# Kernel tuning notes

Measured on AMD Instinct MI355X. Metric: run time of the kernel, lower is better.

Reference implementation:

```python
import jax, jax.numpy as jnp
import numpy as np

S = 4096          # seq_len (longformer-large-4096)
H = 1024          # hidden_size
FF = 3072         # ffnn_size (hardcoded)
G = 100           # number of gold mentions
MAX_SPAN = 30     # max_span_length
TOP_LAMBDA = 0.2
LN_EPS = 1e-5
MASK_VAL = 10000.0


def setup_inputs() -> dict:
    key = jax.random.key(0)
    ks = jax.random.split(key, 16)
    sc = 0.02
    sequence_output = jax.random.normal(ks[0], (1, S, H), jnp.float32)
    attention_mask = jnp.ones((1, S), jnp.int32)
    # valid gold spans: 1 <= start <= end < start + MAX_SPAN (so torch's >0 filter keeps all)
    gs = jax.random.randint(ks[1], (G,), 1, S - MAX_SPAN)
    gl = jax.random.randint(ks[2], (G,), 0, MAX_SPAN)
    gold_mentions = jnp.stack([gs, gs + gl], axis=1).astype(jnp.int32)  # [G, 2]
    inp = {
        'sequence_output': sequence_output,
        'attention_mask': attention_mask,
        'gold_mentions': gold_mentions,
        # start_mention_mlp
        'W_sm': jax.random.normal(ks[3], (H, FF), jnp.float32) * sc,
        'b_sm': jnp.zeros((FF,), jnp.float32),
        'g_sm': jnp.ones((FF,), jnp.float32),
        'beta_sm': jnp.zeros((FF,), jnp.float32),
        # end_mention_mlp
        'W_em': jax.random.normal(ks[4], (H, FF), jnp.float32) * sc,
        'b_em': jnp.zeros((FF,), jnp.float32),
        'g_em': jnp.ones((FF,), jnp.float32),
        'beta_em': jnp.zeros((FF,), jnp.float32),
        # classifiers
        'w_start': jax.random.normal(ks[5], (FF,), jnp.float32) * sc,
        'b_start': jnp.zeros((), jnp.float32),
        'w_end': jax.random.normal(ks[6], (FF,), jnp.float32) * sc,
        'b_end': jnp.zeros((), jnp.float32),
        'W_s2e': jax.random.normal(ks[7], (FF, FF), jnp.float32) * sc,
        'b_s2e': jnp.zeros((FF,), jnp.float32),
    }
    return inp


def _fcl(x, W, b, g, beta):
    # dense -> gelu (exact) -> layernorm (dropout is identity in eval)
    h = jax.nn.gelu(x @ W + b, approximate=False)
    mu = jnp.mean(h, axis=-1, keepdims=True)
    var = jnp.mean(jnp.square(h - mu), axis=-1, keepdims=True)
    return (h - mu) * jax.lax.rsqrt(var + LN_EPS) * g + beta


def _forward(sequence_output, attention_mask, gold_mentions,
             W_sm, b_sm, g_sm, beta_sm, W_em, b_em, g_em, beta_em,
             w_start, b_start, w_end, b_end, W_s2e, b_s2e):
    start_reps = _fcl(sequence_output, W_sm, b_sm, g_sm, beta_sm)  # [1,S,FF]
    end_reps = _fcl(sequence_output, W_em, b_em, g_em, beta_em)    # [1,S,FF]

    start_logits = jnp.einsum('bsf,f->bs', start_reps, w_start) + b_start  # [1,S]
    end_logits = jnp.einsum('bsf,f->bs', end_reps, w_end) + b_end          # [1,S]
    temp = start_reps @ W_s2e + b_s2e                                      # [1,S,FF]
    joint = jnp.einsum('bsf,btf->bst', temp, end_reps)                     # [1,S,S]
    mention_logits = joint + start_logits[:, :, None] + end_logits[:, None, :]

    # span mask: start <= end < start + MAX_SPAN (triu(0) then tril(MAX_SPAN-1))
    i = jnp.arange(S)
    mention_mask = ((i[:, None] <= i[None, :]) & (i[None, :] < i[:, None] + MAX_SPAN)
                    ).astype(jnp.float32)[None]  # [1,S,S]
    mention_logits = jnp.clip(mention_logits + (1.0 - mention_mask) * (-MASK_VAL),
                              -MASK_VAL, MASK_VAL)

    # top-k pruning; attention_mask is full so k is static: int(S * 0.2)
    max_k = int(S * TOP_LAMBDA)  # 819
    _, topk_1d = jax.lax.top_k(mention_logits.reshape(1, -1), max_k)  # [1,max_k]
    sorted_idx = jnp.sort(topk_1d, axis=-1)
    topk_start_ids = sorted_idx // S
    topk_end_ids = sorted_idx % S
    span_mask = jnp.ones((1, max_k), jnp.float32)

    # losses
    probs = jax.nn.sigmoid(mention_logits)  # [1,S,S]
    gstart = gold_mentions[:, 0]
    gend = gold_mentions[:, 1]
    gold_probs = probs[0, gstart, gend]
    # torch BCE clamps log at -100
    cost_gold = -jnp.mean(jnp.maximum(jnp.log(gold_probs), -100.0))
    junk = probs.at[0, gstart, gend].set(0.0)
    log1mp = jnp.maximum(jnp.log(1.0 - junk), -100.0)
    cost_junk = -jnp.sum(jnp.where(mention_mask == 1.0, log1mp, 0.0)) / jnp.sum(mention_mask)
    cost_is_mention = (cost_gold + cost_junk)[None]  # [1]

    return topk_start_ids, topk_end_ids, span_mask, sequence_output, cost_is_mention


def reference(sequence_output, attention_mask, gold_mentions,
              W_sm, b_sm, g_sm, beta_sm, W_em, b_em, g_em, beta_em,
              w_start, b_start, w_end, b_end, W_s2e, b_s2e):
    return _forward(sequence_output, attention_mask, gold_mentions,
                    W_sm, b_sm, g_sm, beta_sm, W_em, b_em, g_em, beta_em,
                    w_start, b_start, w_end, b_end, W_s2e, b_s2e)
```

## Files before the change

### kernel.cpp

```cpp
#include <hip/hip_runtime.h>
#include <math.h>

#define S 4096
#define H 1024
#define FF 3072
#define G 100
#define MAXSPAN 30
#define MAXK 819
#define NBAND (S * MAXSPAN)
#define BAND_COUNT 122445.0

#define O_START 0
#define O_END   819
#define O_MASK  1638
#define O_SEQ   2457
#define O_COST  (2457 + S * H)

typedef __bf16 bf16x8 __attribute__((ext_vector_type(8)));
typedef float f32x16 __attribute__((ext_vector_type(16)));


__device__ __forceinline__ float block_reduce_256(float x, volatile float* red) {
  #pragma unroll
  for (int off = 32; off > 0; off >>= 1) x += __shfl_down(x, off, 64);
  int wid = threadIdx.x >> 6;
  int lane = threadIdx.x & 63;
  __syncthreads();
  if (lane == 0) red[wid] = x;
  __syncthreads();
  return red[0] + red[1] + red[2] + red[3];
}

__device__ __forceinline__ float block_reduce_1024(float x, volatile float* red) {
  #pragma unroll
  for (int off = 32; off > 0; off >>= 1) x += __shfl_down(x, off, 64);
  int wid = threadIdx.x >> 6;
  int lane = threadIdx.x & 63;
  __syncthreads();
  if (lane == 0) red[wid] = x;
  __syncthreads();
  float s = 0.f;
  #pragma unroll
  for (int q = 0; q < 16; q++) s += red[q];
  return s;
}

__device__ __forceinline__ unsigned f2key(float f) {
  unsigned b = __float_as_uint(f);
  return (b & 0x80000000u) ? ~b : (b | 0x80000000u);
}

__device__ __forceinline__ unsigned short bf16_rne(float x) {
  unsigned u = __float_as_uint(x);
  unsigned r = ((u >> 16) & 1u) + 0x7FFFu;
  return (unsigned short)((u + r) >> 16);
}

__device__ __forceinline__ void split2(float x, unsigned short& h, unsigned short& l) {
  h = bf16_rne(x);
  float hf = __uint_as_float(((unsigned)h) << 16);
  l = bf16_rne(x - hf);
}

__device__ __forceinline__ void gld16(const void* g, void* l) {
  __builtin_amdgcn_global_load_lds(
      (const __attribute__((address_space(1))) unsigned int*)g,
      (__attribute__((address_space(3))) unsigned int*)l, 16, 0, 0);
}


__device__ __forceinline__ void pack_a_body(const float* __restrict__ A,
                                            float* __restrict__ Aout,
                                            unsigned short* __restrict__ hi,
                                            unsigned short* __restrict__ lo,
                                            int K, int bx, int by) {
  __shared__ float tile[32][33];
  const int t = threadIdx.x;
  const int tx = t & 31, ty8 = t >> 5;
  const int k0 = bx * 32, r0 = by * 32;
  #pragma unroll
  for (int r = ty8; r < 32; r += 8) {
    float v = A[(size_t)(r0 + r) * K + k0 + tx];
    tile[r][tx] = v;
    if (Aout) Aout[(size_t)(r0 + r) * K + k0 + tx] = v;
  }
  __syncthreads();
  if (t < 128) {
    const int kql = t >> 5;
    const int rl = t & 31;
    unsigned short h8[8], l8[8];
    #pragma unroll
    for (int s = 0; s < 8; s++) split2(tile[rl][kql * 8 + s], h8[s], l8[s]);
    const size_t panel = (size_t)(r0 >> 7);
    const int rloc = (r0 & 127) + rl;
    const size_t off = panel * (size_t)(128 * K) + (size_t)(k0 / 8 + kql) * 1024 + (size_t)rloc * 8;
    *(uint4*)(hi + off) = *(const uint4*)h8;
    *(uint4*)(lo + off) = *(const uint4*)l8;
  }
}

__device__ __forceinline__ void pack_ln_a_body(const float* __restrict__ A,
                                               const float* __restrict__ mu,
                                               const float* __restrict__ rstd,
                                               const float* __restrict__ g,
                                               const float* __restrict__ beta,
                                               unsigned short* __restrict__ hi,
                                               unsigned short* __restrict__ lo,
                                               int K, int bx, int by) {
  __shared__ float tile[32][33];
  const int t = threadIdx.x;
  const int tx = t & 31, ty8 = t >> 5;
  const int k0 = bx * 32, r0 = by * 32;
  #pragma unroll
  for (int r = ty8; r < 32; r += 8)
    tile[r][tx] = A[(size_t)(r0 + r) * K + k0 + tx];
  __syncthreads();
  if (t < 128) {
    const int kql = t >> 5;
    const int rl = t & 31;
    const int row = r0 + rl;
    const float m = mu[row], rs = rstd[row];
    float4 g0 = *(const float4*)(g + k0 + kql * 8);
    float4 g1 = *(const float4*)(g + k0 + kql * 8 + 4);
    float4 b0 = *(const float4*)(beta + k0 + kql * 8);
    float4 b1 = *(const float4*)(beta + k0 + kql * 8 + 4);
    float gv[8] = {g0.x, g0.y, g0.z, g0.w, g1.x, g1.y, g1.z, g1.w};
    float bv[8] = {b0.x, b0.y, b0.z, b0.w, b1.x, b1.y, b1.z, b1.w};
    unsigned short h8[8], l8[8];
    #pragma unroll
    for (int s = 0; s < 8; s++) {
      float v = (tile[rl][kql * 8 + s] - m) * rs * gv[s] + bv[s];
      split2(v, h8[s], l8[s]);
    }
    const size_t panel = (size_t)(r0 >> 7);
    const int rloc = (r0 & 127) + rl;
    const size_t off = panel * (size_t)(128 * K) + (size_t)(k0 / 8 + kql) * 1024 + (size_t)rloc * 8;
    *(uint4*)(hi + off) = *(const uint4*)h8;
    *(uint4*)(lo + off) = *(const uint4*)l8;
  }
}

__device__ __forceinline__ void pack_bt_body(const float* __restrict__ W,
                                             unsigned short* __restrict__ hi,
                                             unsigned short* __restrict__ lo,
                                             int K, int N, int bx, int by) {
  __shared__ float tile[32][33];
  const int t = threadIdx.x;
  const int tx = t & 31, ty8 = t >> 5;
  const int k0 = bx * 32, n0 = by * 32;
  #pragma unroll
  for (int r = ty8; r < 32; r += 8)
    tile[r][tx] = W[(size_t)(k0 + r) * N + n0 + tx];
  __syncthreads();
  if (t < 128) {
    const int kql = t >> 5;
    const int nl = t & 31;
    unsigned short h8[8], l8[8];
    #pragma unroll
    for (int s = 0; s < 8; s++) split2(tile[kql * 8 + s][nl], h8[s], l8[s]);
    const size_t panel = (size_t)(n0 >> 7);
    const int nloc = (n0 & 127) + nl;
    const size_t off = panel * (size_t)(128 * K) + (size_t)(k0 / 8 + kql) * 1024 + (size_t)nloc * 8;
    *(uint4*)(hi + off) = *(const uint4*)h8;
    *(uint4*)(lo + off) = *(const uint4*)l8;
  }
}

__global__ __launch_bounds__(256) void pack_head_kernel(const float* __restrict__ seq,
                                                        float* __restrict__ seq_out,
                                                        unsigned short* __restrict__ sh,
                                                        unsigned short* __restrict__ sl,
                                                        const float* __restrict__ W1,
                                                        const float* __restrict__ W2,
                                                        unsigned short* __restrict__ w1h,
                                                        unsigned short* __restrict__ w1l,
                                                        unsigned short* __restrict__ w2h,
                                                        unsigned short* __restrict__ w2l) {
  const int y = blockIdx.y;
  if (y < 128)      pack_a_body(seq, seq_out, sh, sl, H, blockIdx.x, y);
  else if (y < 224) pack_bt_body(W1, w1h, w1l, H, FF, blockIdx.x, y - 128);
  else              pack_bt_body(W2, w2h, w2l, H, FF, blockIdx.x, y - 224);
}

__global__ __launch_bounds__(256) void pack_mid_kernel(const float* __restrict__ bufS,
                                                       const float* __restrict__ muS,
                                                       const float* __restrict__ rstdS,
                                                       const float* __restrict__ g,
                                                       const float* __restrict__ beta,
                                                       unsigned short* __restrict__ ahi,
                                                       unsigned short* __restrict__ alo,
                                                       const float* __restrict__ Ws2e,
                                                       unsigned short* __restrict__ wbh,
                                                       unsigned short* __restrict__ wbl) {
  const int y = blockIdx.y;
  if (y < 128) pack_ln_a_body(bufS, muS, rstdS, g, beta, ahi, alo, FF, blockIdx.x, y);
  else         pack_bt_body(Ws2e, wbh, wbl, FF, FF, blockIdx.x, y - 128);
}

#define SLOTB 28672
#define A_STR 8192
#define B_BASE 16384
#define B_STR 6144

template <int EPI>
__device__ __forceinline__ void gemm8_body(const char* __restrict__ cAh, const char* __restrict__ cAl,
                                           const char* __restrict__ cBh, const char* __restrict__ cBl,
                                           const float* __restrict__ bias,
                                           float* __restrict__ C,
                                           int bm, int bn, int N, int K,
                                           char* smem) {
  const int tid = threadIdx.x;
  const int lane = tid & 63;
  const int wid = __builtin_amdgcn_readfirstlane(tid >> 6);
  const int wm = wid >> 1, wn = wid & 1;
  const int khalf = lane >> 5;
  const int r31 = lane & 31;
  const size_t PS = (size_t)256 * (size_t)K;

  const char* lsrc[4];
  int ldst[4];
  #pragma unroll
  for (int i = 0; i < 4; i++) { lsrc[i] = cAh; ldst[i] = 0; }
  if (wid < 7) {
    #pragma unroll
    for (int i = 0; i < 4; i++) {
      int q = wid * 4 + i;
      if (q < 16) {
        int str = q >> 3, r = q & 7, kql = r >> 2, u = r & 3;
        lsrc[i] = (str ? cAl : cAh) + (size_t)((bm >> 7) + (u >> 1)) * PS
                + (size_t)(kql * 2048 + (u & 1) * 1024 + lane * 16);
        ldst[i] = str * A_STR + kql * 4096 + u * 1024;
      } else {
        int qq = q - 16;
        int str = qq / 6, r = qq % 6, kql = r / 3, v = r % 3;
        int gcol = bn + 64 * v;
        lsrc[i] = (str ? cBl : cBh) + (size_t)(gcol >> 7) * PS
                + (size_t)(kql * 2048 + ((gcol >> 6) & 1) * 1024 + lane * 16);
        ldst[i] = B_BASE + str * B_STR + kql * 3072 + v * 1024;
      }
    }
  }

  const int aoff = khalf * 4096 + (wm * 64 + r31) * 16;
  const int boff = B_BASE + khalf * 3072 + (wn * 96 + r31) * 16;

  f32x16 acc[2][3];
  #pragma unroll
  for (int mt = 0; mt < 2; mt++)
    #pragma unroll
    for (int nt = 0; nt < 3; nt++)
      #pragma unroll
      for (int r = 0; r < 16; r++) acc[mt][nt][r] = 0.0f;

  auto stage = [&](int h) {
    if (wid < 7) {
      char* sb = smem + (h & 3) * SLOTB;
      const size_t ko = (size_t)h * 4096;
      #pragma unroll
      for (int i = 0; i < 4; i++) gld16(lsrc[i] + ko, sb + ldst[i]);
    }
  };

  const int NH = K >> 4;

  stage(0); stage(1); stage(2);
  asm volatile("s_waitcnt vmcnt(8)" ::: "memory");
  __builtin_amdgcn_s_barrier();

  for (int p = 0; p < NH; ++p) {
    const char* sm = smem + (p & 3) * SLOTB;
    bf16x8 ah[2], al[2], bh[3], bl[3];
    #pragma unroll
    for (int mt = 0; mt < 2; mt++) {
      ah[mt] = *(const bf16x8*)(sm + aoff + mt * 512);
      al[mt] = *(const bf16x8*)(sm + A_STR + aoff + mt * 512);
    }
    #pragma unroll
    for (int nt = 0; nt < 3; nt++) {
      bh[nt] = *(const bf16x8*)(sm + boff + nt * 512);
      bl[nt] = *(const bf16x8*)(sm + B_STR + boff + nt * 512);
    }
    if (p + 3 < NH) stage(p + 3);
    asm volatile("s_waitcnt lgkmcnt(0)" ::: "memory");
    __builtin_amdgcn_s_setprio(1);
    #pragma unroll
    for (int mt = 0; mt < 2; mt++)
      #pragma unroll
      for (int nt = 0; nt < 3; nt++) {
        acc[mt][nt] = __builtin_amdgcn_mfma_f32_32x32x16_bf16(ah[mt], bh[nt], acc[mt][nt], 0, 0, 0);
        acc[mt][nt] = __builtin_amdgcn_mfma_f32_32x32x16_bf16(al[mt], bh[nt], acc[mt][nt], 0, 0, 0);
        acc[mt][nt] = __builtin_amdgcn_mfma_f32_32x32x16_bf16(ah[mt], bl[nt], acc[mt][nt], 0, 0, 0);
      }
    __builtin_amdgcn_s_setprio(0);
    if (p + 4 < NH)       { asm volatile("s_waitcnt vmcnt(8)" ::: "memory"); }
    else if (p + 3 == NH) { asm volatile("s_waitcnt vmcnt(4)" ::: "memory"); }
    else if (p + 2 == NH) { asm volatile("s_waitcnt vmcnt(0)" ::: "memory"); }
    if (p + 1 < NH) __builtin_amdgcn_s_barrier();
  }

  #pragma unroll
  for (int mt = 0; mt < 2; mt++) {
    #pragma unroll
    for (int nt = 0; nt < 3; nt++) {
      const int colg = bn + wn * 96 + nt * 32 + r31;
      const float bb = bias[colg];
      #pragma unroll
      for (int reg = 0; reg < 16; reg++) {
        const int rowl = (reg & 3) + 8 * (reg >> 2) + 4 * khalf;
        const int rowg = bm + wm * 64 + mt * 32 + rowl;
        float v = acc[mt][nt][reg] + bb;
        if (EPI == 1) v = 0.5f * v * (1.0f + erff(v * 0.70710678118654752f));
        C[(size_t)rowg * N + colg] = v;
      }
    }
  }
}

__device__ __forceinline__ void grid_swizzle_16x16(int& bx, int& by) {
  const int lin = blockIdx.y * 16 + blockIdx.x;
  const int X = lin & 7, c = lin >> 3;
  bx = (X & 3) * 4 + (c & 3);
  by = (X >> 2) * 8 + (c >> 2);
}

__global__ __launch_bounds__(512) void gemm_mfma_kernel(const unsigned short* __restrict__ Ahi,
                                                        const unsigned short* __restrict__ Alo,
                                                        const unsigned short* __restrict__ Bhi,
                                                        const unsigned short* __restrict__ Blo,
                                                        const float* __restrict__ bias,
                                                        float* __restrict__ C,
                                                        int N, int K) {
  __shared__ __align__(16) char smem[4 * SLOTB];
  int bx, by;
  grid_swizzle_16x16(bx, by);
  gemm8_body<0>((const char*)Ahi, (const char*)Alo,
                (const char*)Bhi, (const char*)Blo,
                bias, C, by * 256, bx * 192, N, K, smem);
}

__global__ __launch_bounds__(512) void gemm_mfma_dual_kernel(const unsigned short* __restrict__ Ahi,
                                                             const unsigned short* __restrict__ Alo,
                                                             const unsigned short* __restrict__ B1hi,
                                                             const unsigned short* __restrict__ B1lo,
                                                             const unsigned short* __restrict__ B2hi,
                                                             const unsigned short* __restrict__ B2lo,
                                                             const float* __restrict__ bias1,
                                                             const float* __restrict__ bias2,
                                                             float* __restrict__ C1,
                                                             float* __restrict__ C2,
                                                             int N, int K) {
  __shared__ __align__(16) char smem[4 * SLOTB];
  const int zb = blockIdx.z;
  const unsigned short* Bhi = zb ? B2hi : B1hi;
  const unsigned short* Blo = zb ? B2lo : B1lo;
  const float* bias = zb ? bias2 : bias1;
  float* C = zb ? C2 : C1;
  int bx, by;
  grid_swizzle_16x16(bx, by);
  gemm8_body<1>((const char*)Ahi, (const char*)Alo,
                (const char*)Bhi, (const char*)Blo,
                bias, C, by * 256, bx * 192, N, K, smem);
}


__global__ __launch_bounds__(256) void ln_stats_kernel(const float* __restrict__ HbS,
                                                       const float* __restrict__ HbE,
                                                       const float* __restrict__ gS,
                                                       const float* __restrict__ betaS,
                                                       const float* __restrict__ wS,
                                                       const float* __restrict__ bS,
                                                       const float* __restrict__ gE,
                                                       const float* __restrict__ betaE,
                                                       const float* __restrict__ wE,
                                                       const float* __restrict__ bE,
                                                       float* __restrict__ slog,
                                                       float* __restrict__ elog,
                                                       float* __restrict__ muS,
                                                       float* __restrict__ rstdS,
                                                       float* __restrict__ muE,
                                                       float* __restrict__ rstdE) {
  __shared__ float red[4];
  const int row = blockIdx.x, tid = threadIdx.x;
  const int br = blockIdx.y;
  const float* Hb = br ? HbE : HbS;
  const float* g = br ? gE : gS;
  const float* beta = br ? betaE : betaS;
  const float* w = br ? wE : wS;
  const float* bsc = br ? bE : bS;
  const float* h = Hb + (size_t)row * FF;

  float4 v[3];
  float s = 0.0f;
  #pragma unroll
  for (int t = 0; t < 3; t++) {
    v[t] = *(const float4*)(h + tid * 4 + t * 1024);
    s += v[t].x + v[t].y + v[t].z + v[t].w;
  }
  float mu = block_reduce_256(s, red) * (1.0f / (float)FF);

  float s2 = 0.0f;
  #pragma unroll
  for (int t = 0; t < 3; t++) {
    float dx = v[t].x - mu, dy = v[t].y - mu, dz = v[t].z - mu, dw = v[t].w - mu;
    s2 += dx * dx + dy * dy + dz * dz + dw * dw;
  }
  float var = block_reduce_256(s2, red) * (1.0f / (float)FF);
  float rstd = rsqrtf(var + 1e-5f);

  float dot = 0.0f;
  #pragma unroll
  for (int t = 0; t < 3; t++) {
    int idx = tid * 4 + t * 1024;
    float4 gv = *(const float4*)(g + idx);
    float4 bv = *(const float4*)(beta + idx);
    float4 wv = *(const float4*)(w + idx);
    float rx = (v[t].x - mu) * rstd * gv.x + bv.x;
    float ry = (v[t].y - mu) * rstd * gv.y + bv.y;
    float rz = (v[t].z - mu) * rstd * gv.z + bv.z;
    float rw = (v[t].w - mu) * rstd * gv.w + bv.w;
    dot += rx * wv.x + ry * wv.y + rz * wv.z + rw * wv.w;
  }
  float dt = block_reduce_256(dot, red);
  if (tid == 0) {
    if (br) { elog[row] = dt + bsc[0]; muE[row] = mu; rstdE[row] = rstd; }
    else    { slog[row] = dt + bsc[0]; muS[row] = mu; rstdS[row] = rstd; }
  }
}


__global__ __launch_bounds__(256) void band_joint_kernel(const float* __restrict__ T,
                                                         const float* __restrict__ Eraw,
                                                         const float* __restrict__ muE,
                                                         const float* __restrict__ rstdE,
                                                         const float* __restrict__ gE,
                                                         const float* __restrict__ betaE,
                                                         const float* __restrict__ sl,
                                                         const float* __restrict__ el,
                                                         float* __restrict__ band,
                                                         double* __restrict__ jacc,
                                                         unsigned* __restrict__ hist16) {
  __shared__ float Elds[45][260];
  __shared__ float red[4];
  const int t = threadIdx.x;
  const int bx = blockIdx.x;
  const int sbx = (bx & 7) * 32 + (bx >> 3);
  const int i0 = sbx * 16;
  const int r_l = t >> 4, c = t & 15;

  float accd[MAXSPAN];
  #pragma unroll
  for (int d = 0; d < MAXSPAN; d++) accd[d] = 0.0f;

  for (int k0 = 0; k0 < FF; k0 += 256) {
    const float* trow = T + (size_t)(i0 + r_l) * FF + k0 + c * 16;
    float4 tv0 = *(const float4*)(trow + 0);
    float4 tv1 = *(const float4*)(trow + 4);
    float4 tv2 = *(const float4*)(trow + 8);
    float4 tv3 = *(const float4*)(trow + 12);
    __syncthreads();
    for (int rr = t >> 6; rr < 45; rr += 4) {
      int gr = i0 + rr;
      int cc = (t & 63) * 4;
      float4 rv = {0.f, 0.f, 0.f, 0.f};
      if (gr < S) {
        float4 ev = *(const float4*)(Eraw + (size_t)gr * FF + k0 + cc);
        float m = muE[gr], rs = rstdE[gr];
        float4 gv = *(const float4*)(gE + k0 + cc);
        float4 bv = *(const float4*)(betaE + k0 + cc);
        rv.x = (ev.x - m) * rs * gv.x + bv.x;
        rv.y = (ev.y - m) * rs * gv.y + bv.y;
        rv.z = (ev.z - m) * rs * gv.z + bv.z;
        rv.w = (ev.w - m) * rs * gv.w + bv.w;
      }
      *(float4*)&Elds[rr][cc] = rv;
    }
    __syncthreads();
    #pragma unroll
    for (int d = 0; d < MAXSPAN; d++) {
      const float* er = &Elds[r_l + d][c * 16];
      float4 e0 = *(const float4*)(er + 0);
      float4 e1 = *(const float4*)(er + 4);
      float4 e2 = *(const float4*)(er + 8);
      float4 e3 = *(const float4*)(er + 12);
      accd[d] += tv0.x * e0.x + tv0.y * e0.y + tv0.z * e0.z + tv0.w * e0.w
               + tv1.x * e1.x + tv1.y * e1.y + tv1.z * e1.z + tv1.w * e1.w
               + tv2.x * e2.x + tv2.y * e2.y + tv2.z * e2.z + tv2.w * e2.w
               + tv3.x * e3.x + tv3.y * e3.y + tv3.z * e3.z + tv3.w * e3.w;
    }
  }

  const int i = i0 + r_l;
  const float my_sl = sl[i];
  float jsum = 0.0f;
  #pragma unroll
  for (int d = 0; d < MAXSPAN; d++) {
    float v = accd[d];
    v += __shfl_down(v, 8, 16);
    v += __shfl_down(v, 4, 16);
    v += __shfl_down(v, 2, 16);
    v += __shfl_down(v, 1, 16);
    if (c == 0) {
      int j = i + d;
      if (j < S) {
        float vv = v + my_sl + el[j];
        vv = fminf(fmaxf(vv, -10000.0f), 10000.0f);
        band[i * MAXSPAN + d] = vv;
        atomicAdd(&hist16[f2key(vv) >> 16], 1u);
        float p = 1.0f / (1.0f + expf(-vv));
        jsum += fmaxf(logf(1.0f - p), -100.0f);
      } else {
        band[i * MAXSPAN + d] = -1e30f;
      }
    }
  }
  float tot = block_reduce_256(jsum, red);
  if (t == 0) atomicAdd(jacc, (double)tot);
}


__global__ __launch_bounds__(1024) void topk_finalize_kernel(const float* __restrict__ band,
                                                             const int* __restrict__ gold,
                                                             const double* __restrict__ jacc,
                                                             const unsigned* __restrict__ hist16,
                                                             float* __restrict__ out) {
  __shared__ int csum[1024];
  __shared__ unsigned sh_T16;
  __shared__ int sh_remk;
  __shared__ int sh_chunk, sh_above;
  __shared__ int idxbuf[1024];
  __shared__ unsigned tkey[256];
  __shared__ int tidx[256];
  __shared__ int cnt_gt, cnt_eq;
  __shared__ int sb[1024];
  __shared__ int gcell[G];
  __shared__ float redf[16];
  const int tid = threadIdx.x;

  int s = 0;
  #pragma unroll 8
  for (int q = 0; q < 64; q++) s += (int)hist16[tid * 64 + q];
  csum[tid] = s;
  __syncthreads();
  for (int off = 1; off < 1024; off <<= 1) {
    int v = (tid + off < 1024) ? csum[tid + off] : 0;
    __syncthreads();
    csum[tid] += v;
    __syncthreads();
  }
  {
    int nxt = (tid < 1023) ? csum[tid + 1] : 0;
    if (csum[tid] >= MAXK && nxt < MAXK) { sh_chunk = tid; sh_above = nxt; }
  }
  __syncthreads();
  if (tid == 0) {
    int cum = sh_above;
    int b = sh_chunk * 64 + 63;
    for (;; b--) {
      int h = (int)hist16[b];
      if (cum + h >= MAXK || b == sh_chunk * 64) { sh_T16 = (unsigned)b; sh_remk = MAXK - cum; break; }
      cum += h;
    }
  }
  __syncthreads();
  const unsigned T16 = sh_T16;
  int remk = sh_remk;

  if (tid == 0) { cnt_gt = 0; cnt_eq = 0; }
  __syncthreads();
  for (int e = tid; e < NBAND; e += 1024) {
    unsigned key = f2key(band[e]);
    unsigned k16 = key >> 16;
    if (k16 >= T16) {
      int i = e / MAXSPAN, d = e - i * MAXSPAN;
      int fi = i * S + i + d;
      if (k16 > T16) {
        int p = atomicAdd(&cnt_gt, 1);
        if (p < 1024) idxbuf[p] = fi;
      } else {
        int p = atomicAdd(&cnt_eq, 1);
        if (p < 256) { tkey[p] = key; tidx[p] = fi; }
      }
    }
  }
  __syncthreads();
  if (tid == 0) {
    int ngt = cnt_gt < 1024 ? cnt_gt : 1024;
    int ne = cnt_eq < 256 ? cnt_eq : 256;
    for (int a2 = 1; a2 < ne; a2++) {
      unsigned kv = tkey[a2]; int iv = tidx[a2];
      int b2 = a2 - 1;
      while (b2 >= 0 && (tkey[b2] < kv || (tkey[b2] == kv && tidx[b2] > iv))) {
        tkey[b2 + 1] = tkey[b2]; tidx[b2 + 1] = tidx[b2]; b2--;
      }
      tkey[b2 + 1] = kv; tidx[b2 + 1] = iv;
    }
    int take = remk < ne ? remk : ne;
    for (int q = 0; q < take; q++)
      if (ngt + q < 1024) idxbuf[ngt + q] = tidx[q];
  }
  __syncthreads();

  sb[tid] = (tid < MAXK) ? idxbuf[tid] : 0x7FFFFFFF;
  __syncthreads();
  for (int ksz = 2; ksz <= 1024; ksz <<= 1) {
    for (int jj = ksz >> 1; jj > 0; jj >>= 1) {
      int ixj = tid ^ jj;
      if (ixj > tid) {
        int a2 = sb[tid], b2 = sb[ixj];
        bool up = ((tid & ksz) == 0);
        if (up ? (a2 > b2) : (a2 < b2)) { sb[tid] = b2; sb[ixj] = a2; }
      }
      __syncthreads();
    }
  }
  if (tid < MAXK) {
    int fi = sb[tid];
    out[O_START + tid] = (float)(fi >> 12);
    out[O_END + tid]   = (float)(fi & 4095);
    out[O_MASK + tid]  = 1.0f;
  }

  if (tid < G) {
    int gs = gold[2 * tid], ge = gold[2 * tid + 1];
    gcell[tid] = gs * MAXSPAN + (ge - gs);
  }
  __syncthreads();
  float tg = 0.0f, tj = 0.0f;
  if (tid < G) {
    int cell = gcell[tid];
    float x = band[cell];
    float p = 1.0f / (1.0f + expf(-x));
    tg = fmaxf(logf(p), -100.0f);
    bool first = true;
    for (int q = 0; q < tid; q++)
      if (gcell[q] == cell) { first = false; break; }
    if (first) tj = fmaxf(logf(1.0f - p), -100.0f);
  }
  float sg = block_reduce_1024(tg, redf);
  float sj = block_reduce_1024(tj, redf);
  if (tid == 0) {
    double junk = *jacc - (double)sj;
    double cost = -((double)sg / (double)G) - (junk / BAND_COUNT);
    out[O_COST] = (float)cost;
  }
}


extern "C" void kernel_launch(void* const* d_in, const int* in_sizes, int n_in,
                              void* d_out, int out_size, void* d_ws, size_t ws_size,
                              hipStream_t stream) {
  (void)in_sizes; (void)n_in; (void)out_size; (void)ws_size;
  const float* seq    = (const float*)d_in[0];
  const int*   gold   = (const int*)d_in[2];
  const float* W_sm   = (const float*)d_in[3];
  const float* b_sm   = (const float*)d_in[4];
  const float* g_sm   = (const float*)d_in[5];
  const float* be_sm  = (const float*)d_in[6];
  const float* W_em   = (const float*)d_in[7];
  const float* b_em   = (const float*)d_in[8];
  const float* g_em   = (const float*)d_in[9];
  const float* be_em  = (const float*)d_in[10];
  const float* w_st   = (const float*)d_in[11];
  const float* b_st   = (const float*)d_in[12];
  const float* w_en   = (const float*)d_in[13];
  const float* b_en   = (const float*)d_in[14];
  const float* W_s2e  = (const float*)d_in[15];
  const float* b_s2e  = (const float*)d_in[16];
  float* out = (float*)d_out;
  char* ws = (char*)d_ws;

  const size_t SZ_REP = (size_t)S * FF * 4;
  float*  bufS = (float*)(ws);
  float*  bufE = (float*)(ws + SZ_REP);
  float*  bufT = (float*)(ws + 2 * SZ_REP);
  char* R3 = ws + 3 * SZ_REP;
  unsigned short* seqhi = (unsigned short*)R3;
  unsigned short* seqlo = (unsigned short*)(R3 + (size_t)S * H * 2);
  unsigned short* a3hi  = (unsigned short*)R3;
  unsigned short* a3lo  = (unsigned short*)(R3 + (size_t)S * FF * 2);
  char* R4 = ws + 4 * SZ_REP;
  const size_t SZ_W12 = (size_t)H * FF * 2;
  unsigned short* wb1hi = (unsigned short*)R4;
  unsigned short* wb1lo = (unsigned short*)(R4 + SZ_W12);
  unsigned short* wb2hi = (unsigned short*)(R4 + 2 * SZ_W12);
  unsigned short* wb2lo = (unsigned short*)(R4 + 3 * SZ_W12);
  unsigned short* wbhi = (unsigned short*)R4;
  unsigned short* wblo = (unsigned short*)(R4 + (size_t)FF * FF * 2);
  char* R5 = R4 + 2 * (size_t)FF * FF * 2;
  float*    band   = (float*)R5;
  unsigned* hist16 = (unsigned*)(R5 + (size_t)NBAND * 4);
  double*   jacc   = (double*)(R5 + (size_t)NBAND * 4 + 262144);
  float*    slog   = (float*)(R5 + (size_t)NBAND * 4 + 262144 + 64);
  float*  elog  = slog + S;
  float*  muS   = elog + S;
  float*  rstdS = muS + S;
  float*  muE   = rstdS + S;
  float*  rstdE = muE + S;

  hipMemsetAsync(hist16, 0, 262144 + 64 + 8, stream);

  dim3 gg(16, 16);
  dim3 gg2(16, 16, 2);

  pack_head_kernel<<<dim3(32, 320), 256, 0, stream>>>(seq, out + O_SEQ, seqhi, seqlo,
                                                      W_sm, W_em, wb1hi, wb1lo, wb2hi, wb2lo);
  gemm_mfma_dual_kernel<<<gg2, 512, 0, stream>>>(seqhi, seqlo, wb1hi, wb1lo, wb2hi, wb2lo,
                                                 b_sm, b_em, bufS, bufE, FF, H);
  ln_stats_kernel<<<dim3(S, 2), 256, 0, stream>>>(bufS, bufE, g_sm, be_sm, w_st, b_st,
                                                  g_em, be_em, w_en, b_en,
                                                  slog, elog, muS, rstdS, muE, rstdE);
  pack_mid_kernel<<<dim3(96, 224), 256, 0, stream>>>(bufS, muS, rstdS, g_sm, be_sm,
                                                     a3hi, a3lo, W_s2e, wbhi, wblo);
  gemm_mfma_kernel<<<gg, 512, 0, stream>>>(a3hi, a3lo, wbhi, wblo, b_s2e, bufT, FF, FF);

  band_joint_kernel<<<S / 16, 256, 0, stream>>>(bufT, bufE, muE, rstdE, g_em, be_em,
                                                slog, elog, band, jacc, hist16);

  topk_finalize_kernel<<<1, 1024, 0, stream>>>(band, gold, jacc, hist16, out);
}
```

Measured before the change: 785.5 us.

## Double-buffer LDS fragment registers in GEMM main loop to overlap reads with MFMA

Restructures the bf16x3 split GEMM main loop to unroll by two, using two sets of fragment registers. LDS reads for the next k-step are issued before the MFMAs of the current step, and a sched_barrier keeps that order. The global-load wait counts and barriers are reworked so the 4-slot ring still stays correct. This aims to hide LDS latency behind matrix ops, at the cost of more VGPRs and more fragile wait logic; it also assumes NH is even.

Result: no change. 773.4 us (-1.6%).

```diff
diff --git a/kernel.cpp b/kernel.cpp
--- a/kernel.cpp
+++ b/kernel.cpp
@@ -201,6 +201,34 @@
 #define A_STR 8192
 #define B_BASE 16384
 #define B_STR 6144
+
+#define LOAD_FRAGS(P1, AH, AL, BH, BL) do {                      \
+    const char* sm_ = smem + ((P1) & 3) * SLOTB;                 \
+    AH[0] = *(const bf16x8*)(sm_ + aoff);                        \
+    AH[1] = *(const bf16x8*)(sm_ + aoff + 512);                  \
+    BH[0] = *(const bf16x8*)(sm_ + boff);                        \
+    BH[1] = *(const bf16x8*)(sm_ + boff + 512);                  \
+    BH[2] = *(const bf16x8*)(sm_ + boff + 1024);                 \
+    AL[0] = *(const bf16x8*)(sm_ + A_STR + aoff);                \
+    AL[1] = *(const bf16x8*)(sm_ + A_STR + aoff + 512);          \
+    BL[0] = *(const bf16x8*)(sm_ + B_STR + boff);                \
+    BL[1] = *(const bf16x8*)(sm_ + B_STR + boff + 512);          \
+    BL[2] = *(const bf16x8*)(sm_ + B_STR + boff + 1024);         \
+  } while (0)
+
+#define MFMA_ONE(MT, NT, AH, AL, BH, BL)                                                              \
+    acc[MT][NT] = __builtin_amdgcn_mfma_f32_32x32x16_bf16(AH[MT], BH[NT], acc[MT][NT], 0, 0, 0);      \
+    acc[MT][NT] = __builtin_amdgcn_mfma_f32_32x32x16_bf16(AL[MT], BH[NT], acc[MT][NT], 0, 0, 0);      \
+    acc[MT][NT] = __builtin_amdgcn_mfma_f32_32x32x16_bf16(AH[MT], BL[NT], acc[MT][NT], 0, 0, 0);
+
+#define MFMA_SET(AH, AL, BH, BL) do {   \
+    MFMA_ONE(0, 0, AH, AL, BH, BL)      \
+    MFMA_ONE(0, 1, AH, AL, BH, BL)      \
+    MFMA_ONE(0, 2, AH, AL, BH, BL)      \
+    MFMA_ONE(1, 0, AH, AL, BH, BL)      \
+    MFMA_ONE(1, 1, AH, AL, BH, BL)      \
+    MFMA_ONE(1, 2, AH, AL, BH, BL)      \
+  } while (0)
 
 template <int EPI>
 __device__ __forceinline__ void gemm8_body(const char* __restrict__ cAh, const char* __restrict__ cAl,
@@ -263,39 +291,34 @@
 
   const int NH = K >> 4;
 
+  bf16x8 ahA[2], alA[2], bhA[3], blA[3];
+  bf16x8 ahB[2], alB[2], bhB[3], blB[3];
+
   stage(0); stage(1); stage(2);
-  asm volatile("s_waitcnt vmcnt(8)" ::: "memory");
-  __builtin_amdgcn_s_barrier();
-
-  for (int p = 0; p < NH; ++p) {
-    const char* sm = smem + (p & 3) * SLOTB;
-    bf16x8 ah[2], al[2], bh[3], bl[3];
-    #pragma unroll
-    for (int mt = 0; mt < 2; mt++) {
-      ah[mt] = *(const bf16x8*)(sm + aoff + mt * 512);
-      al[mt] = *(const bf16x8*)(sm + A_STR + aoff + mt * 512);
-    }
-    #pragma unroll
-    for (int nt = 0; nt < 3; nt++) {
-      bh[nt] = *(const bf16x8*)(sm + boff + nt * 512);
-      bl[nt] = *(const bf16x8*)(sm + B_STR + boff + nt * 512);
-    }
+  asm volatile("s_waitcnt vmcnt(4)" ::: "memory");
+  asm volatile("s_barrier" ::: "memory");
+  LOAD_FRAGS(0, ahA, alA, bhA, blA);
+
+  for (int p = 0; p < NH; p += 2) {
     if (p + 3 < NH) stage(p + 3);
-    asm volatile("s_waitcnt lgkmcnt(0)" ::: "memory");
+    LOAD_FRAGS(p + 1, ahB, alB, bhB, blB);
+    __builtin_amdgcn_sched_barrier(0);
     __builtin_amdgcn_s_setprio(1);
-    #pragma unroll
-    for (int mt = 0; mt < 2; mt++)
-      #pragma unroll
-      for (int nt = 0; nt < 3; nt++) {
-        acc[mt][nt] = __builtin_amdgcn_mfma_f32_32x32x16_bf16(ah[mt], bh[nt], acc[mt][nt], 0, 0, 0);
-        acc[mt][nt] = __builtin_amdgcn_mfma_f32_32x32x16_bf16(al[mt], bh[nt], acc[mt][nt], 0, 0, 0);
-        acc[mt][nt] = __builtin_amdgcn_mfma_f32_32x32x16_bf16(ah[mt], bl[nt], acc[mt][nt], 0, 0, 0);
-      }
+    MFMA_SET(ahA, alA, bhA, blA);
     __builtin_amdgcn_s_setprio(0);
-    if (p + 4 < NH)       { asm volatile("s_waitcnt vmcnt(8)" ::: "memory"); }
-    else if (p + 3 == NH) { asm volatile("s_waitcnt vmcnt(4)" ::: "memory"); }
-    else if (p + 2 == NH) { asm volatile("s_waitcnt vmcnt(0)" ::: "memory"); }
-    if (p + 1 < NH) __builtin_amdgcn_s_barrier();
+    if (p + 3 < NH)       { asm volatile("s_waitcnt vmcnt(4)" ::: "memory"); }
+    else if (p + 3 == NH) { asm volatile("s_waitcnt vmcnt(0)" ::: "memory"); }
+    if (p + 2 < NH) asm volatile("s_barrier" ::: "memory");
+
+    if (p + 4 < NH) stage(p + 4);
+    if (p + 2 < NH) LOAD_FRAGS(p + 2, ahA, alA, bhA, blA);
+    __builtin_amdgcn_sched_barrier(0);
+    __builtin_amdgcn_s_setprio(1);
+    MFMA_SET(ahB, alB, bhB, blB);
+    __builtin_amdgcn_s_setprio(0);
+    if (p + 4 < NH)       { asm volatile("s_waitcnt vmcnt(4)" ::: "memory"); }
+    else if (p + 4 == NH) { asm volatile("s_waitcnt vmcnt(0)" ::: "memory"); }
+    if (p + 3 < NH) asm volatile("s_barrier" ::: "memory");
   }
 
   #pragma unroll
```
